# Kernel tuning notes

Hardware: AMD Instinct MI355X
Metric: run time of the kernel (lower is better)

The kernel has to match this reference:

```python
import jax, jax.numpy as jnp
import numpy as np

D_MODEL = 1024
NUM_TILES = 64
TPC = 8                 # tiles per cluster
NC = NUM_TILES // TPC   # num clusters = 8
GRID = 16
CH = D_MODEL // 4       # compress hidden = 256
EPS_LN = 1e-5


def setup_inputs() -> dict:
    key = jax.random.key(0)
    ks = jax.random.split(key, 8)
    B, T = 8, 4096
    x = jax.random.normal(ks[0], (B, T, D_MODEL), dtype=jnp.float32)
    gamma = jnp.ones((D_MODEL,), jnp.float32)
    beta = jnp.zeros((D_MODEL,), jnp.float32)
    W1 = jax.random.normal(ks[1], (CH, D_MODEL), jnp.float32) * 0.02
    b1 = jnp.zeros((CH,), jnp.float32)
    W2 = jax.random.normal(ks[2], (2, CH), jnp.float32) * 0.02
    b2 = jnp.zeros((2,), jnp.float32)
    spline_coeffs = jax.random.normal(ks[3], (NUM_TILES, GRID, GRID, 3), jnp.float32) * 0.5
    spline_scales = jnp.ones((NUM_TILES,), jnp.float32)
    directions = jax.random.normal(ks[4], (NUM_TILES, D_MODEL), jnp.float32) * 0.02
    output_scale = jnp.ones((), jnp.float32) * 0.1
    return {"x": x, "gamma": gamma, "beta": beta, "W1": W1, "b1": b1,
            "W2": W2, "b2": b2, "spline_coeffs": spline_coeffs,
            "spline_scales": spline_scales, "directions": directions,
            "output_scale": output_scale}


def _forward(x, gamma, beta, W1, b1, W2, b2, spline_coeffs, spline_scales,
             directions, output_scale):
    B, T, D = x.shape
    N = B * T
    # LayerNorm
    mu = jnp.mean(x, axis=-1, keepdims=True)
    var = jnp.mean((x - mu) ** 2, axis=-1, keepdims=True)
    x_norm = (x - mu) / jnp.sqrt(var + EPS_LN) * gamma + beta
    xf = x_norm.reshape(N, D)

    # routing signatures
    sigs = jnp.sign(directions)                                  # [NT, D]
    cluster_sigs = jnp.sign(sigs.reshape(NC, TPC, D).mean(axis=1))  # [NC, D]

    # hierarchical routing: cluster argmax then tile argmax within cluster
    cluster_idx = jnp.argmax(xf @ cluster_sigs.T, axis=-1)       # [N]
    tile_scores = (xf @ sigs.T).reshape(N, NC, TPC)              # [N, NC, TPC]
    sel = jnp.take_along_axis(tile_scores, cluster_idx[:, None, None], axis=1)[:, 0, :]
    local_idx = jnp.argmax(sel, axis=-1)                         # [N]
    tile_idx = cluster_idx * TPC + local_idx                     # cluster tiles are contiguous

    # shared compression -> (a, b) in [-1, 1]
    h = jax.nn.gelu(xf @ W1.T + b1, approximate=False)
    comp = jnp.tanh(h @ W2.T + b2)                               # [N, 2]
    a, b = comp[:, 0], comp[:, 1]

    # ternary quantized spline coefficients (STE forward value)
    q = jnp.where(spline_coeffs > 0.3, 1.0,
                  jnp.where(spline_coeffs < -0.3, -1.0, 0.0))
    qc = spline_coeffs + jax.lax.stop_gradient(q - spline_coeffs)  # [NT, G, G, 3]

    idx_a = jnp.clip(((a + 1) / 2 * GRID).astype(jnp.int32), 0, GRID - 1)
    idx_b = jnp.clip(((b + 1) / 2 * GRID).astype(jnp.int32), 0, GRID - 1)
    cell = qc[tile_idx, idx_a, idx_b]                            # [N, 3]
    cell_size = 2.0 / GRID
    local_a = (a + 1 - idx_a.astype(jnp.float32) * cell_size) / cell_size
    local_b = (b + 1 - idx_b.astype(jnp.float32) * cell_size) / cell_size
    spline_val = cell[:, 0] + cell[:, 1] * local_a + cell[:, 2] * local_b
    scale_val = spline_val * spline_scales[tile_idx]             # [N]

    out = scale_val[:, None] * directions[tile_idx]              # [N, D]
    out = out.reshape(B, T, D) * output_scale
    output = x + out                                             # dropout is identity in eval

    # load-balance aux loss
    counts = jax.ops.segment_sum(jnp.ones((N,), jnp.float32), tile_idx,
                                 num_segments=NUM_TILES)
    ideal = N / NUM_TILES
    balance = jnp.mean((counts - ideal) ** 2) / (ideal ** 2 + 1e-8) * 0.01
    return output, tile_idx.reshape(B, T), comp.reshape(B, T, 2), balance


def reference(x, gamma, beta, W1, b1, W2, b2, spline_coeffs, spline_scales,
              directions, output_scale):
    return _forward(x, gamma, beta, W1, b1, W2, b2, spline_coeffs,
                    spline_scales, directions, output_scale)
```

## Files before the change

### kernel.cpp

```cpp
#include <hip/hip_runtime.h>

#define D_MODEL 1024
#define ROWS    32
#define BT      1024
#define EPS_LN  1e-5f

typedef _Float16 f16x8 __attribute__((ext_vector_type(8)));
typedef float    f32x4 __attribute__((ext_vector_type(4)));

#define WS_CNT   0
#define WS_B1P   256
#define WS_CT    1280
#define WS_FH    4096
#define WS_FL    (4096 + 688128)
#define WS_NEED  (4096 + 2 * 688128)


__global__ void prep_kernel(const float* __restrict__ W1,
                            const float* __restrict__ dirs,
                            const float* __restrict__ gamma,
                            const float* __restrict__ beta,
                            const float* __restrict__ b1,
                            char* __restrict__ wsb, int useT) {
    const int b = blockIdx.x, tid = threadIdx.x;
    if (b < 168) {
        if (!useT) return;
        const int gid = b * 256 + tid;
        const int ct = gid >> 11, ks = (gid >> 6) & 31, l = gid & 63;
        const int c16 = l & 15, kb = ks * 32 + ((l >> 4) << 3);
        f16x8 h, lo;
#pragma unroll
        for (int i = 0; i < 8; ++i) {
            const int k = kb + i;
            const float g = gamma[k];
            float v;
            if (ct < 16) {
                v = g * W1[(ct * 16 + c16) * 1024 + k];
            } else if (ct < 20) {
                const float d = dirs[((ct - 16) * 16 + c16) * 1024 + k];
                v = g * (float)((d > 0.f) - (d < 0.f));
            } else {
                if (c16 < 8) {
                    int s = 0;
                    for (int t = 0; t < 8; ++t) {
                        const float d = dirs[(c16 * 8 + t) * 1024 + k];
                        s += (d > 0.f) - (d < 0.f);
                    }
                    v = g * (float)((s > 0) - (s < 0));
                } else v = 0.f;
            }
            const _Float16 hh = (_Float16)v;
            h[i] = hh; lo[i] = (_Float16)(v - (float)hh);
        }
        *(f16x8*)(wsb + WS_FH + (size_t)gid * 16) = h;
        *(f16x8*)(wsb + WS_FL + (size_t)gid * 16) = lo;
    } else if (b < 184) {
        __shared__ float red[256];
        const int jl = tid >> 4, sub = tid & 15;
        const int j = (b - 168) * 16 + jl;
        float s = 0.f;
        for (int i = 0; i < 64; ++i) {
            const int k = sub * 64 + i;
            s += beta[k] * W1[j * 1024 + k];
        }
        red[tid] = s;
        __syncthreads();
        if (sub == 0) {
            float t = 0.f;
            for (int p = 0; p < 16; ++p) t += red[jl * 16 + p];
            ((float*)(wsb + WS_B1P))[j] = b1[j] + t;
        }
    } else if (b < 192) {
        const int t8 = (b - 184) * 8 + (tid >> 5), l32 = tid & 31;
        float s = 0.f;
        for (int i = 0; i < 32; ++i) {
            const int k = l32 * 32 + i;
            const float d = dirs[t8 * 1024 + k];
            s += beta[k] * (float)((d > 0.f) - (d < 0.f));
        }
        s += __shfl_xor(s, 1); s += __shfl_xor(s, 2); s += __shfl_xor(s, 4);
        s += __shfl_xor(s, 8); s += __shfl_xor(s, 16);
        if (l32 == 0) ((float*)(wsb + WS_CT))[t8] = s;
    } else if (b == 192) {
        const int c = tid >> 5, l32 = tid & 31;
        float s = 0.f;
        for (int i = 0; i < 32; ++i) {
            const int k = l32 * 32 + i;
            int ss = 0;
            for (int t = 0; t < 8; ++t) {
                const float d = dirs[(c * 8 + t) * 1024 + k];
                ss += (d > 0.f) - (d < 0.f);
            }
            s += beta[k] * (float)((ss > 0) - (ss < 0));
        }
        s += __shfl_xor(s, 1); s += __shfl_xor(s, 2); s += __shfl_xor(s, 4);
        s += __shfl_xor(s, 8); s += __shfl_xor(s, 16);
        if (l32 == 0) ((float*)(wsb + WS_CT))[64 + c] = s;
    } else {
        if (tid < 64) ((unsigned*)(wsb + WS_CNT))[tid] = 0u;
        else if (tid < 72) ((float*)(wsb + WS_CT))[72 + (tid - 64)] = 0.f;
    }
}

template <int USET, int NT, int CT0>
__device__ __forceinline__ void loadBW(const char* __restrict__ wsb,
                                       const float* __restrict__ W1,
                                       const float* __restrict__ gamma,
                                       int ks, int ln, f16x8* bh, f16x8* bl) {
    if (USET) {
        const size_t fo = ((size_t)((CT0 * 32 + ks) * 64 + ln)) * 16;
#pragma unroll
        for (int t = 0; t < NT; ++t) {
            bh[t] = *(const f16x8*)(wsb + WS_FH + fo + (size_t)t * 32 * 64 * 16);
            bl[t] = *(const f16x8*)(wsb + WS_FL + fo + (size_t)t * 32 * 64 * 16);
        }
    } else {
        const int c16 = ln & 15, kb = ks * 32 + ((ln >> 4) << 3);
#pragma unroll
        for (int t = 0; t < NT; ++t) {
#pragma unroll
            for (int i = 0; i < 8; ++i) {
                const int k = kb + i;
                const float v = gamma[k] * W1[((CT0 + t) * 16 + c16) * 1024 + k];
                const _Float16 hh = (_Float16)v;
                bh[t][i] = hh; bl[t][i] = (_Float16)(v - (float)hh);
            }
        }
    }
}

template <int USET, int CT0>
__device__ __forceinline__ f16x8 loadBS(const char* __restrict__ wsb,
                                        const float* __restrict__ dirs,
                                        const float* __restrict__ gamma,
                                        int ks, int ln) {
    if (USET) {
        return *(const f16x8*)(wsb + WS_FH + ((size_t)((CT0 * 32 + ks) * 64 + ln)) * 16);
    }
    const int c16 = ln & 15, kb = ks * 32 + ((ln >> 4) << 3);
    f16x8 s;
#pragma unroll
    for (int i = 0; i < 8; ++i) {
        const int k = kb + i;
        float v;
        if (CT0 < 20) {
            const float d = dirs[((CT0 - 16) * 16 + c16) * 1024 + k];
            v = gamma[k] * (float)((d > 0.f) - (d < 0.f));
        } else {
            if (c16 < 8) {
                int ss = 0;
                for (int tt = 0; tt < 8; ++tt) {
                    const float d = dirs[(c16 * 8 + tt) * 1024 + k];
                    ss += (d > 0.f) - (d < 0.f);
                }
                v = gamma[k] * (float)((ss > 0) - (ss < 0));
            } else v = 0.f;
        }
        s[i] = (_Float16)v;
    }
    return s;
}

template <int NT>
__device__ __forceinline__ void mfma3p(const f16x8 (&a)[2][2], const f16x8* bh,
                                       const f16x8* bl, f32x4 (*acc)[2]) {
    __builtin_amdgcn_s_setprio(1);
#pragma unroll
    for (int t = 0; t < NT; ++t) {
        acc[t][0] = __builtin_amdgcn_mfma_f32_16x16x32_f16(a[0][0], bh[t], acc[t][0], 0, 0, 0);
        acc[t][1] = __builtin_amdgcn_mfma_f32_16x16x32_f16(a[1][0], bh[t], acc[t][1], 0, 0, 0);
    }
#pragma unroll
    for (int t = 0; t < NT; ++t) {
        acc[t][0] = __builtin_amdgcn_mfma_f32_16x16x32_f16(a[0][0], bl[t], acc[t][0], 0, 0, 0);
        acc[t][1] = __builtin_amdgcn_mfma_f32_16x16x32_f16(a[1][0], bl[t], acc[t][1], 0, 0, 0);
    }
#pragma unroll
    for (int t = 0; t < NT; ++t) {
        acc[t][0] = __builtin_amdgcn_mfma_f32_16x16x32_f16(a[0][1], bh[t], acc[t][0], 0, 0, 0);
        acc[t][1] = __builtin_amdgcn_mfma_f32_16x16x32_f16(a[1][1], bh[t], acc[t][1], 0, 0, 0);
    }
    __builtin_amdgcn_s_setprio(0);
}

#define LDA2(KS, A) { const int cc_ = (((KS) * 32 + kofs) ^ asw); \
                      const int i0_ = r16 * 1024 + cc_, i1_ = (16 + r16) * 1024 + cc_; \
                      A[0][0] = *(const f16x8*)&xh[i0_]; A[0][1] = *(const f16x8*)&xl[i0_]; \
                      A[1][0] = *(const f16x8*)&xh[i1_]; A[1][1] = *(const f16x8*)&xl[i1_]; }

template <int USET, int NT, int CT0>
__device__ __forceinline__ void runW(const _Float16* __restrict__ xh,
                                     const _Float16* __restrict__ xl,
                                     const char* __restrict__ wsb,
                                     const float* __restrict__ W1,
                                     const float* __restrict__ gamma,
                                     const float* __restrict__ W2,
                                     int wv, int ln, float (*part)[32][2]) {
    const int r16 = ln & 15, kgrp = ln >> 4;
    const int kofs = kgrp << 3, asw = (r16 & 7) << 3;
    const float* b1p = (const float*)(wsb + WS_B1P);

    f32x4 acc[NT][2];
#pragma unroll
    for (int t = 0; t < NT; ++t) {
        acc[t][0] = (f32x4){0.f, 0.f, 0.f, 0.f};
        acc[t][1] = (f32x4){0.f, 0.f, 0.f, 0.f};
    }
    f16x8 bh0[NT], bl0[NT], bh1[NT], bl1[NT];
    f16x8 a0[2][2], a1[2][2];

    loadBW<USET, NT, CT0>(wsb, W1, gamma, 0, ln, bh0, bl0);
    LDA2(0, a0);
    for (int ks = 0; ks < 32; ks += 2) {
        loadBW<USET, NT, CT0>(wsb, W1, gamma, ks + 1, ln, bh1, bl1);
        LDA2(ks + 1, a1);
        mfma3p<NT>(a0, bh0, bl0, acc);
        if (ks + 2 < 32) {
            loadBW<USET, NT, CT0>(wsb, W1, gamma, ks + 2, ln, bh0, bl0);
            LDA2(ks + 2, a0);
        }
        mfma3p<NT>(a1, bh1, bl1, acc);
    }

    float p0s[2][4] = {{0.f,0.f,0.f,0.f},{0.f,0.f,0.f,0.f}};
    float p1s[2][4] = {{0.f,0.f,0.f,0.f},{0.f,0.f,0.f,0.f}};
#pragma unroll
    for (int t = 0; t < NT; ++t) {
        const int col = (CT0 + t) * 16 + r16;
        const float b1c = b1p[col], w20 = W2[col], w21 = W2[256 + col];
#pragma unroll
        for (int rt = 0; rt < 2; ++rt)
#pragma unroll
            for (int reg = 0; reg < 4; ++reg) {
                const float h = acc[t][rt][reg] + b1c;
                const float gl = 0.5f * h * (1.f + erff(h * 0.70710678118654752f));
                p0s[rt][reg] += gl * w20; p1s[rt][reg] += gl * w21;
            }
    }
#pragma unroll
    for (int rt = 0; rt < 2; ++rt)
#pragma unroll
        for (int reg = 0; reg < 4; ++reg) {
            float v0 = p0s[rt][reg], v1 = p1s[rt][reg];
            v0 += __shfl_xor(v0, 1); v0 += __shfl_xor(v0, 2);
            v0 += __shfl_xor(v0, 4); v0 += __shfl_xor(v0, 8);
            v1 += __shfl_xor(v1, 1); v1 += __shfl_xor(v1, 2);
            v1 += __shfl_xor(v1, 4); v1 += __shfl_xor(v1, 8);
            if (r16 == 0) {
                const int row = rt * 16 + kgrp * 4 + reg;
                part[wv][row][0] = v0; part[wv][row][1] = v1;
            }
        }
}

template <int USET, int CT0>
__device__ __forceinline__ void runS(const _Float16* __restrict__ xh,
                                     const _Float16* __restrict__ xl,
                                     const char* __restrict__ wsb,
                                     const float* __restrict__ dirs,
                                     const float* __restrict__ gamma,
                                     int ln, float (*scores)[84]) {
    const int r16 = ln & 15, kgrp = ln >> 4;
    const int kofs = kgrp << 3, asw = (r16 & 7) << 3;
    const float* ctv = (const float*)(wsb + WS_CT);

    f32x4 acc[2];
    acc[0] = (f32x4){0.f, 0.f, 0.f, 0.f};
    acc[1] = (f32x4){0.f, 0.f, 0.f, 0.f};
    f16x8 bh0, bh1;
    f16x8 a0[2][2], a1[2][2];

    bh0 = loadBS<USET, CT0>(wsb, dirs, gamma, 0, ln);
    LDA2(0, a0);
    for (int ks = 0; ks < 32; ks += 2) {
        bh1 = loadBS<USET, CT0>(wsb, dirs, gamma, ks + 1, ln);
        LDA2(ks + 1, a1);
        __builtin_amdgcn_s_setprio(1);
        acc[0] = __builtin_amdgcn_mfma_f32_16x16x32_f16(a0[0][0], bh0, acc[0], 0, 0, 0);
        acc[1] = __builtin_amdgcn_mfma_f32_16x16x32_f16(a0[1][0], bh0, acc[1], 0, 0, 0);
        acc[0] = __builtin_amdgcn_mfma_f32_16x16x32_f16(a0[0][1], bh0, acc[0], 0, 0, 0);
        acc[1] = __builtin_amdgcn_mfma_f32_16x16x32_f16(a0[1][1], bh0, acc[1], 0, 0, 0);
        __builtin_amdgcn_s_setprio(0);
        if (ks + 2 < 32) {
            bh0 = loadBS<USET, CT0>(wsb, dirs, gamma, ks + 2, ln);
            LDA2(ks + 2, a0);
        }
        __builtin_amdgcn_s_setprio(1);
        acc[0] = __builtin_amdgcn_mfma_f32_16x16x32_f16(a1[0][0], bh1, acc[0], 0, 0, 0);
        acc[1] = __builtin_amdgcn_mfma_f32_16x16x32_f16(a1[1][0], bh1, acc[1], 0, 0, 0);
        acc[0] = __builtin_amdgcn_mfma_f32_16x16x32_f16(a1[0][1], bh1, acc[0], 0, 0, 0);
        acc[1] = __builtin_amdgcn_mfma_f32_16x16x32_f16(a1[1][1], bh1, acc[1], 0, 0, 0);
        __builtin_amdgcn_s_setprio(0);
    }

    const int sc = (CT0 - 16) * 16 + r16;
    const float cadd = ctv[sc];
#pragma unroll
    for (int rt = 0; rt < 2; ++rt)
#pragma unroll
        for (int reg = 0; reg < 4; ++reg)
            scores[rt * 16 + kgrp * 4 + reg][sc] = acc[rt][reg] + cadd;
}

template <int USET>
__launch_bounds__(BT, 1)
__global__ void main_kernel(const float* __restrict__ x,
                            const float* __restrict__ gamma,
                            const float* __restrict__ beta,
                            const float* __restrict__ W1,
                            const float* __restrict__ b1,
                            const float* __restrict__ W2,
                            const float* __restrict__ b2,
                            const float* __restrict__ spline,
                            const float* __restrict__ sscale,
                            const float* __restrict__ dirs,
                            const float* __restrict__ oscale,
                            float* __restrict__ out,
                            float* __restrict__ out_tile,
                            float* __restrict__ out_comp,
                            char* __restrict__ wsb) {
    __shared__ __align__(16) _Float16 xh[ROWS * 1024];
    __shared__ __align__(16) _Float16 xl[ROWS * 1024];
    __shared__ float scores[ROWS][84];
    __shared__ float part[11][ROWS][2];
    __shared__ float mu_s[ROWS], sstd_s[ROWS];
    __shared__ float sval_s[ROWS];
    __shared__ int   tidx_s[ROWS];

    const int tid = threadIdx.x, wv = tid >> 6, ln = tid & 63;
    const int row0 = blockIdx.x * ROWS;

    for (int q = 0; q < 2; ++q) {
        const int rl = wv * 2 + q;
        const float4* xp = (const float4*)(x + (size_t)(row0 + rl) * D_MODEL);
        float4 xa[2][2];
        xa[0][0] = xp[2 * ln];       xa[0][1] = xp[2 * ln + 1];
        xa[1][0] = xp[2 * ln + 128]; xa[1][1] = xp[2 * ln + 129];
        float s = 0.f;
#pragma unroll
        for (int g = 0; g < 2; ++g)
#pragma unroll
            for (int j = 0; j < 2; ++j)
                s += xa[g][j].x + xa[g][j].y + xa[g][j].z + xa[g][j].w;
#pragma unroll
        for (int o = 1; o < 64; o <<= 1) s += __shfl_xor(s, o);
        const float mu = s * (1.f / 1024.f);
        float v = 0.f;
#pragma unroll
        for (int g = 0; g < 2; ++g)
#pragma unroll
            for (int j = 0; j < 2; ++j) {
                float dx;
                dx = xa[g][j].x - mu; v += dx * dx;
                dx = xa[g][j].y - mu; v += dx * dx;
                dx = xa[g][j].z - mu; v += dx * dx;
                dx = xa[g][j].w - mu; v += dx * dx;
            }
#pragma unroll
        for (int o = 1; o < 64; o <<= 1) v += __shfl_xor(v, o);
        const float sstd = sqrtf(v * (1.f / 1024.f) + EPS_LN);
        const float rstd = 1.f / sstd;
        if (ln == 0) { mu_s[rl] = mu; sstd_s[rl] = sstd; }
        const int sw = (rl & 7) << 3;
#pragma unroll
        for (int g = 0; g < 2; ++g) {
            const float f[8] = {xa[g][0].x, xa[g][0].y, xa[g][0].z, xa[g][0].w,
                                xa[g][1].x, xa[g][1].y, xa[g][1].z, xa[g][1].w};
            f16x8 hv, lv;
#pragma unroll
            for (int i = 0; i < 8; ++i) {
                const float o0 = (f[i] - mu) * rstd;
                const _Float16 t0 = (_Float16)o0;
                hv[i] = t0; lv[i] = (_Float16)(o0 - (float)t0);
            }
            const int idx = rl * 1024 + ((8 * ln + 512 * g) ^ sw);
            *(f16x8*)&xh[idx] = hv;
            *(f16x8*)&xl[idx] = lv;
        }
    }
    __syncthreads();

    if (wv == 0)       runW<USET, 2, 0 >(xh, xl, wsb, W1, gamma, W2, wv, ln, part);
    else if (wv == 1)  runW<USET, 2, 2 >(xh, xl, wsb, W1, gamma, W2, wv, ln, part);
    else if (wv == 2)  runW<USET, 2, 4 >(xh, xl, wsb, W1, gamma, W2, wv, ln, part);
    else if (wv == 3)  runW<USET, 2, 6 >(xh, xl, wsb, W1, gamma, W2, wv, ln, part);
    else if (wv == 4)  runW<USET, 2, 8 >(xh, xl, wsb, W1, gamma, W2, wv, ln, part);
    else if (wv == 5)  runW<USET, 1, 10>(xh, xl, wsb, W1, gamma, W2, wv, ln, part);
    else if (wv == 6)  runW<USET, 1, 11>(xh, xl, wsb, W1, gamma, W2, wv, ln, part);
    else if (wv == 7)  runW<USET, 1, 12>(xh, xl, wsb, W1, gamma, W2, wv, ln, part);
    else if (wv == 8)  runW<USET, 1, 13>(xh, xl, wsb, W1, gamma, W2, wv, ln, part);
    else if (wv == 9)  runW<USET, 1, 14>(xh, xl, wsb, W1, gamma, W2, wv, ln, part);
    else if (wv == 10) runW<USET, 1, 15>(xh, xl, wsb, W1, gamma, W2, wv, ln, part);
    else if (wv == 11) runS<USET, 16>(xh, xl, wsb, dirs, gamma, ln, scores);
    else if (wv == 12) runS<USET, 17>(xh, xl, wsb, dirs, gamma, ln, scores);
    else if (wv == 13) runS<USET, 18>(xh, xl, wsb, dirs, gamma, ln, scores);
    else if (wv == 14) runS<USET, 19>(xh, xl, wsb, dirs, gamma, ln, scores);
    else               runS<USET, 20>(xh, xl, wsb, dirs, gamma, ln, scores);
    __syncthreads();

    unsigned* cntp = (unsigned*)(wsb + WS_CNT);
    if (tid < ROWS) {
        const int r = tid;
        float c0v = b2[0], c1v = b2[1];
#pragma unroll
        for (int w = 0; w < 11; ++w) { c0v += part[w][r][0]; c1v += part[w][r][1]; }
        const float a = tanhf(c0v), b = tanhf(c1v);
        out_comp[(size_t)(row0 + r) * 2 + 0] = a;
        out_comp[(size_t)(row0 + r) * 2 + 1] = b;

        int bc = 0; float bs = scores[r][64];
#pragma unroll
        for (int c = 1; c < 8; ++c) { const float v = scores[r][64 + c]; if (v > bs) { bs = v; bc = c; } }
        int bt = 0; float ts = scores[r][bc * 8];
#pragma unroll
        for (int p = 1; p < 8; ++p) { const float v = scores[r][bc * 8 + p]; if (v > ts) { ts = v; bt = p; } }
        const int ti = bc * 8 + bt;
        tidx_s[r] = ti;
        atomicAdd(&cntp[ti], 1u);
        out_tile[row0 + r] = (float)ti;

        int ia = (int)((a + 1.0f) / 2.0f * 16.0f);
        int ib = (int)((b + 1.0f) / 2.0f * 16.0f);
        ia = min(max(ia, 0), 15); ib = min(max(ib, 0), 15);
        const float* cp = spline + ((ti * 16 + ia) * 16 + ib) * 3;
        float c0 = cp[0], c1 = cp[1], c2 = cp[2];
        c0 = (c0 > 0.3f) ? 1.f : ((c0 < -0.3f) ? -1.f : 0.f);
        c1 = (c1 > 0.3f) ? 1.f : ((c1 < -0.3f) ? -1.f : 0.f);
        c2 = (c2 > 0.3f) ? 1.f : ((c2 < -0.3f) ? -1.f : 0.f);
        const float la = (a + 1.0f - (float)ia * 0.125f) * 8.0f;
        const float lb = (b + 1.0f - (float)ib * 0.125f) * 8.0f;
        sval_s[r] = (c0 + c1 * la + c2 * lb) * sscale[ti];
    }
    __syncthreads();

    const float os = oscale[0];
    for (int q = 0; q < 2; ++q) {
        const int rl = wv * 2 + q, row = row0 + rl;
        const int ti = tidx_s[rl];
        const float s = sval_s[rl] * os;
        const float mu = mu_s[rl], sd = sstd_s[rl];
        const int sw = (rl & 7) << 3;
        const float4* dp = (const float4*)(dirs + (size_t)ti * D_MODEL);
        float4* op = (float4*)(out + (size_t)row * D_MODEL);
#pragma unroll
        for (int g = 0; g < 2; ++g) {
            const int idx = rl * 1024 + ((8 * ln + 512 * g) ^ sw);
            const f16x8 hv = *(const f16x8*)&xh[idx];
            const f16x8 lv = *(const f16x8*)&xl[idx];
            const float4 d0 = dp[2 * ln + 128 * g];
            const float4 d1 = dp[2 * ln + 1 + 128 * g];
            float4 o0, o1;
            o0.x = ((float)hv[0] + (float)lv[0]) * sd + mu + s * d0.x;
            o0.y = ((float)hv[1] + (float)lv[1]) * sd + mu + s * d0.y;
            o0.z = ((float)hv[2] + (float)lv[2]) * sd + mu + s * d0.z;
            o0.w = ((float)hv[3] + (float)lv[3]) * sd + mu + s * d0.w;
            o1.x = ((float)hv[4] + (float)lv[4]) * sd + mu + s * d1.x;
            o1.y = ((float)hv[5] + (float)lv[5]) * sd + mu + s * d1.y;
            o1.z = ((float)hv[6] + (float)lv[6]) * sd + mu + s * d1.z;
            o1.w = ((float)hv[7] + (float)lv[7]) * sd + mu + s * d1.w;
            op[2 * ln + 128 * g] = o0;
            op[2 * ln + 1 + 128 * g] = o1;
        }
    }
}

__global__ void bal_kernel(const unsigned* __restrict__ counts, float* __restrict__ ob) {
    const int t = threadIdx.x;
    const float d = (float)counts[t] - 512.0f;
    float v = d * d;
#pragma unroll
    for (int o = 1; o < 64; o <<= 1) v += __shfl_xor(v, o);
    if (t == 0) ob[0] = (v * (1.f / 64.f)) / 262144.0f * 0.01f;
}

extern "C" void kernel_launch(void* const* d_in, const int* in_sizes, int n_in,
                              void* d_out, int out_size, void* d_ws, size_t ws_size,
                              hipStream_t stream) {
    const float* x      = (const float*)d_in[0];
    const float* gamma  = (const float*)d_in[1];
    const float* beta   = (const float*)d_in[2];
    const float* W1     = (const float*)d_in[3];
    const float* b1     = (const float*)d_in[4];
    const float* W2     = (const float*)d_in[5];
    const float* b2     = (const float*)d_in[6];
    const float* spline = (const float*)d_in[7];
    const float* sscale = (const float*)d_in[8];
    const float* dirs   = (const float*)d_in[9];
    const float* oscale = (const float*)d_in[10];

    const int nrows = in_sizes[0] / D_MODEL;
    float* out      = (float*)d_out;
    float* out_tile = out + (size_t)nrows * D_MODEL;
    float* out_comp = out_tile + nrows;
    float* out_bal  = out_comp + (size_t)nrows * 2;

    char* wsb = (char*)d_ws;
    const int useT = (ws_size >= (size_t)WS_NEED) ? 1 : 0;

    prep_kernel<<<194, 256, 0, stream>>>(W1, dirs, gamma, beta, b1, wsb, useT);
    if (useT)
        main_kernel<1><<<nrows / ROWS, BT, 0, stream>>>(x, gamma, beta, W1, b1, W2, b2,
                                                        spline, sscale, dirs, oscale,
                                                        out, out_tile, out_comp, wsb);
    else
        main_kernel<0><<<nrows / ROWS, BT, 0, stream>>>(x, gamma, beta, W1, b1, W2, b2,
                                                        spline, sscale, dirs, oscale,
                                                        out, out_tile, out_comp, wsb);
    bal_kernel<<<1, 64, 0, stream>>>((const unsigned*)(wsb + WS_CNT), out_bal);
}
```

Before: 174.2 us.

## Halve rows per block to 16 and drop manual double-buffered MFMA pipeline

Reduces the per-block row tile from 32 to 16, so each wave handles one row and one 16-row MFMA tile. This halves the LDS footprint and accumulator registers, and the launch-bounds hint is raised to allow more resident blocks per CU. The explicit software prefetch (double-buffered A/B fragments) is removed in favour of a simple per-k-step load-then-MFMA loop. The trade-off is that weight fragments are now reused across only half as many rows, which doubles weight traffic, and latency hiding now relies on occupancy rather than manual pipelining.

```diff
diff --git a/kernel.cpp b/kernel.cpp
--- a/kernel.cpp
+++ b/kernel.cpp
@@ -1,7 +1,7 @@
 #include <hip/hip_runtime.h>
 
 #define D_MODEL 1024
-#define ROWS    32
+#define ROWS    16
 #define BT      1024
 #define EPS_LN  1e-5f
 
@@ -161,32 +161,9 @@
     return s;
 }
 
-template <int NT>
-__device__ __forceinline__ void mfma3p(const f16x8 (&a)[2][2], const f16x8* bh,
-                                       const f16x8* bl, f32x4 (*acc)[2]) {
-    __builtin_amdgcn_s_setprio(1);
-#pragma unroll
-    for (int t = 0; t < NT; ++t) {
-        acc[t][0] = __builtin_amdgcn_mfma_f32_16x16x32_f16(a[0][0], bh[t], acc[t][0], 0, 0, 0);
-        acc[t][1] = __builtin_amdgcn_mfma_f32_16x16x32_f16(a[1][0], bh[t], acc[t][1], 0, 0, 0);
-    }
-#pragma unroll
-    for (int t = 0; t < NT; ++t) {
-        acc[t][0] = __builtin_amdgcn_mfma_f32_16x16x32_f16(a[0][0], bl[t], acc[t][0], 0, 0, 0);
-        acc[t][1] = __builtin_amdgcn_mfma_f32_16x16x32_f16(a[1][0], bl[t], acc[t][1], 0, 0, 0);
-    }
-#pragma unroll
-    for (int t = 0; t < NT; ++t) {
-        acc[t][0] = __builtin_amdgcn_mfma_f32_16x16x32_f16(a[0][1], bh[t], acc[t][0], 0, 0, 0);
-        acc[t][1] = __builtin_amdgcn_mfma_f32_16x16x32_f16(a[1][1], bh[t], acc[t][1], 0, 0, 0);
-    }
-    __builtin_amdgcn_s_setprio(0);
-}
-
-#define LDA2(KS, A) { const int cc_ = (((KS) * 32 + kofs) ^ asw); \
-                      const int i0_ = r16 * 1024 + cc_, i1_ = (16 + r16) * 1024 + cc_; \
-                      A[0][0] = *(const f16x8*)&xh[i0_]; A[0][1] = *(const f16x8*)&xl[i0_]; \
-                      A[1][0] = *(const f16x8*)&xh[i1_]; A[1][1] = *(const f16x8*)&xl[i1_]; }
+#define LDA1(KS) { const int cc_ = (((KS) * 32 + kofs) ^ asw); \
+                   const int i0_ = r16 * 1024 + cc_; \
+                   ah = *(const f16x8*)&xh[i0_]; al = *(const f16x8*)&xl[i0_]; }
 
 template <int USET, int NT, int CT0>
 __device__ __forceinline__ void runW(const _Float16* __restrict__ xh,
@@ -195,62 +172,57 @@
                                      const float* __restrict__ W1,
                                      const float* __restrict__ gamma,
                                      const float* __restrict__ W2,
-                                     int wv, int ln, float (*part)[32][2]) {
+                                     int wv, int ln, float (*part)[ROWS][2]) {
     const int r16 = ln & 15, kgrp = ln >> 4;
     const int kofs = kgrp << 3, asw = (r16 & 7) << 3;
     const float* b1p = (const float*)(wsb + WS_B1P);
 
-    f32x4 acc[NT][2];
-#pragma unroll
-    for (int t = 0; t < NT; ++t) {
-        acc[t][0] = (f32x4){0.f, 0.f, 0.f, 0.f};
-        acc[t][1] = (f32x4){0.f, 0.f, 0.f, 0.f};
-    }
-    f16x8 bh0[NT], bl0[NT], bh1[NT], bl1[NT];
-    f16x8 a0[2][2], a1[2][2];
-
-    loadBW<USET, NT, CT0>(wsb, W1, gamma, 0, ln, bh0, bl0);
-    LDA2(0, a0);
-    for (int ks = 0; ks < 32; ks += 2) {
-        loadBW<USET, NT, CT0>(wsb, W1, gamma, ks + 1, ln, bh1, bl1);
-        LDA2(ks + 1, a1);
-        mfma3p<NT>(a0, bh0, bl0, acc);
-        if (ks + 2 < 32) {
-            loadBW<USET, NT, CT0>(wsb, W1, gamma, ks + 2, ln, bh0, bl0);
-            LDA2(ks + 2, a0);
-        }
-        mfma3p<NT>(a1, bh1, bl1, acc);
-    }
-
-    float p0s[2][4] = {{0.f,0.f,0.f,0.f},{0.f,0.f,0.f,0.f}};
-    float p1s[2][4] = {{0.f,0.f,0.f,0.f},{0.f,0.f,0.f,0.f}};
+    f32x4 acc[NT];
+#pragma unroll
+    for (int t = 0; t < NT; ++t) acc[t] = (f32x4){0.f, 0.f, 0.f, 0.f};
+
+    for (int ks = 0; ks < 32; ++ks) {
+        f16x8 bh[NT], bl[NT], ah, al;
+        loadBW<USET, NT, CT0>(wsb, W1, gamma, ks, ln, bh, bl);
+        LDA1(ks);
+        __builtin_amdgcn_s_setprio(1);
+#pragma unroll
+        for (int t = 0; t < NT; ++t)
+            acc[t] = __builtin_amdgcn_mfma_f32_16x16x32_f16(ah, bh[t], acc[t], 0, 0, 0);
+#pragma unroll
+        for (int t = 0; t < NT; ++t)
+            acc[t] = __builtin_amdgcn_mfma_f32_16x16x32_f16(ah, bl[t], acc[t], 0, 0, 0);
+#pragma unroll
+        for (int t = 0; t < NT; ++t)
+            acc[t] = __builtin_amdgcn_mfma_f32_16x16x32_f16(al, bh[t], acc[t], 0, 0, 0);
+        __builtin_amdgcn_s_setprio(0);
+    }
+
+    float p0s[4] = {0.f, 0.f, 0.f, 0.f};
+    float p1s[4] = {0.f, 0.f, 0.f, 0.f};
 #pragma unroll
     for (int t = 0; t < NT; ++t) {
         const int col = (CT0 + t) * 16 + r16;
         const float b1c = b1p[col], w20 = W2[col], w21 = W2[256 + col];
 #pragma unroll
-        for (int rt = 0; rt < 2; ++rt)
-#pragma unroll
-            for (int reg = 0; reg < 4; ++reg) {
-                const float h = acc[t][rt][reg] + b1c;
-                const float gl = 0.5f * h * (1.f + erff(h * 0.70710678118654752f));
-                p0s[rt][reg] += gl * w20; p1s[rt][reg] += gl * w21;
-            }
-    }
-#pragma unroll
-    for (int rt = 0; rt < 2; ++rt)
-#pragma unroll
         for (int reg = 0; reg < 4; ++reg) {
-            float v0 = p0s[rt][reg], v1 = p1s[rt][reg];
-            v0 += __shfl_xor(v0, 1); v0 += __shfl_xor(v0, 2);
-            v0 += __shfl_xor(v0, 4); v0 += __shfl_xor(v0, 8);
-            v1 += __shfl_xor(v1, 1); v1 += __shfl_xor(v1, 2);
-            v1 += __shfl_xor(v1, 4); v1 += __shfl_xor(v1, 8);
-            if (r16 == 0) {
-                const int row = rt * 16 + kgrp * 4 + reg;
-                part[wv][row][0] = v0; part[wv][row][1] = v1;
-            }
-        }
+            const float h = acc[t][reg] + b1c;
+            const float gl = 0.5f * h * (1.f + erff(h * 0.70710678118654752f));
+            p0s[reg] += gl * w20; p1s[reg] += gl * w21;
+        }
+    }
+#pragma unroll
+    for (int reg = 0; reg < 4; ++reg) {
+        float v0 = p0s[reg], v1 = p1s[reg];
+        v0 += __shfl_xor(v0, 1); v0 += __shfl_xor(v0, 2);
+        v0 += __shfl_xor(v0, 4); v0 += __shfl_xor(v0, 8);
+        v1 += __shfl_xor(v1, 1); v1 += __shfl_xor(v1, 2);
+        v1 += __shfl_xor(v1, 4); v1 += __shfl_xor(v1, 8);
+        if (r16 == 0) {
+            const int row = kgrp * 4 + reg;
+            part[wv][row][0] = v0; part[wv][row][1] = v1;
+        }
+    }
 }
 
 template <int USET, int CT0>
@@ -264,46 +236,26 @@
     const int kofs = kgrp << 3, asw = (r16 & 7) << 3;
     const float* ctv = (const float*)(wsb + WS_CT);
 
-    f32x4 acc[2];
-    acc[0] = (f32x4){0.f, 0.f, 0.f, 0.f};
-    acc[1] = (f32x4){0.f, 0.f, 0.f, 0.f};
-    f16x8 bh0, bh1;
-    f16x8 a0[2][2], a1[2][2];
-
-    bh0 = loadBS<USET, CT0>(wsb, dirs, gamma, 0, ln);
-    LDA2(0, a0);
-    for (int ks = 0; ks < 32; ks += 2) {
-        bh1 = loadBS<USET, CT0>(wsb, dirs, gamma, ks + 1, ln);
-        LDA2(ks + 1, a1);
+    f32x4 acc = (f32x4){0.f, 0.f, 0.f, 0.f};
+    for (int ks = 0; ks < 32; ++ks) {
+        f16x8 ah, al;
+        const f16x8 bh = loadBS<USET, CT0>(wsb, dirs, gamma, ks, ln);
+        LDA1(ks);
         __builtin_amdgcn_s_setprio(1);
-        acc[0] = __builtin_amdgcn_mfma_f32_16x16x32_f16(a0[0][0], bh0, acc[0], 0, 0, 0);
-        acc[1] = __builtin_amdgcn_mfma_f32_16x16x32_f16(a0[1][0], bh0, acc[1], 0, 0, 0);
-        acc[0] = __builtin_amdgcn_mfma_f32_16x16x32_f16(a0[0][1], bh0, acc[0], 0, 0, 0);
-        acc[1] = __builtin_amdgcn_mfma_f32_16x16x32_f16(a0[1][1], bh0, acc[1], 0, 0, 0);
-        __builtin_amdgcn_s_setprio(0);
-        if (ks + 2 < 32) {
-            bh0 = loadBS<USET, CT0>(wsb, dirs, gamma, ks + 2, ln);
-            LDA2(ks + 2, a0);
-        }
-        __builtin_amdgcn_s_setprio(1);
-        acc[0] = __builtin_amdgcn_mfma_f32_16x16x32_f16(a1[0][0], bh1, acc[0], 0, 0, 0);
-        acc[1] = __builtin_amdgcn_mfma_f32_16x16x32_f16(a1[1][0], bh1, acc[1], 0, 0, 0);
-        acc[0] = __builtin_amdgcn_mfma_f32_16x16x32_f16(a1[0][1], bh1, acc[0], 0, 0, 0);
-        acc[1] = __builtin_amdgcn_mfma_f32_16x16x32_f16(a1[1][1], bh1, acc[1], 0, 0, 0);
+        acc = __builtin_amdgcn_mfma_f32_16x16x32_f16(ah, bh, acc, 0, 0, 0);
+        acc = __builtin_amdgcn_mfma_f32_16x16x32_f16(al, bh, acc, 0, 0, 0);
         __builtin_amdgcn_s_setprio(0);
     }
 
     const int sc = (CT0 - 16) * 16 + r16;
     const float cadd = ctv[sc];
 #pragma unroll
-    for (int rt = 0; rt < 2; ++rt)
-#pragma unroll
-        for (int reg = 0; reg < 4; ++reg)
-            scores[rt * 16 + kgrp * 4 + reg][sc] = acc[rt][reg] + cadd;
+    for (int reg = 0; reg < 4; ++reg)
+        scores[kgrp * 4 + reg][sc] = acc[reg] + cadd;
 }
 
 template <int USET>
-__launch_bounds__(BT, 1)
+__launch_bounds__(BT, 8)
 __global__ void main_kernel(const float* __restrict__ x,
                             const float* __restrict__ gamma,
                             const float* __restrict__ beta,
@@ -330,8 +282,8 @@
     const int tid = threadIdx.x, wv = tid >> 6, ln = tid & 63;
     const int row0 = blockIdx.x * ROWS;
 
-    for (int q = 0; q < 2; ++q) {
-        const int rl = wv * 2 + q;
+    {
+        const int rl = wv;
         const float4* xp = (const float4*)(x + (size_t)(row0 + rl) * D_MODEL);
         float4 xa[2][2];
         xa[0][0] = xp[2 * ln];       xa[0][1] = xp[2 * ln + 1];
@@ -434,8 +386,8 @@
     __syncthreads();
 
     const float os = oscale[0];
-    for (int q = 0; q < 2; ++q) {
-        const int rl = wv * 2 + q, row = row0 + rl;
+    {
+        const int rl = wv, row = row0 + rl;
         const int ti = tidx_s[rl];
         const float s = sval_s[rl] * os;
         const float mu = mu_s[rl], sd = sstd_s[rl];
```

Measured after the change: 178.5 us. 1.02x slower.
